# Performance work log

Hardware: AMD Instinct MI355X
Metric: run time of the kernel (lower is better)

Reference implementation:

```python
import jax, jax.numpy as jnp
import numpy as np

B, S, HID = 2, 2048, 4096
NH, NKV, D = 32, 8, 128  # heads, kv heads, head_dim
GROUPS = NH // NKV
THETA = 10000.0


def _rope_tables():
    inv_freq = 1.0 / (THETA ** (np.arange(0, D, 2, dtype=np.float32) / D))
    pos = np.arange(S, dtype=np.float32)
    freqs = pos[:, None] * inv_freq[None, :]          # [S, D/2]
    emb = np.concatenate([freqs, freqs], axis=-1)      # [S, D]
    cos = np.broadcast_to(np.cos(emb)[None], (B, S, D)).copy()
    sin = np.broadcast_to(np.sin(emb)[None], (B, S, D)).copy()
    return jnp.asarray(cos), jnp.asarray(sin)


def setup_inputs() -> dict:
    key = jax.random.key(0)
    ks = jax.random.split(key, 5)
    hidden_states = jax.random.normal(ks[0], (B, S, HID), dtype=jnp.float32)
    cos, sin = _rope_tables()
    std = 0.02
    Wq = jax.random.normal(ks[1], (NH * D, HID), dtype=jnp.float32) * std
    Wk = jax.random.normal(ks[2], (NKV * D, HID), dtype=jnp.float32) * std
    Wv = jax.random.normal(ks[3], (NKV * D, HID), dtype=jnp.float32) * std
    Wo = jax.random.normal(ks[4], (HID, NH * D), dtype=jnp.float32) * std
    return {"hidden_states": hidden_states, "cos": cos, "sin": sin,
            "Wq": Wq, "Wk": Wk, "Wv": Wv, "Wo": Wo}


def _rotate_half(x):
    x1, x2 = jnp.split(x, 2, axis=-1)
    return jnp.concatenate([-x2, x1], axis=-1)


def reference(hidden_states, cos, sin, Wq, Wk, Wv, Wo):
    b, s, _ = hidden_states.shape
    # QKV projections (no bias; attention_bias=False)
    q = (hidden_states @ Wq.T).reshape(b, s, NH, D).transpose(0, 2, 1, 3)    # [B,NH,S,D]
    k = (hidden_states @ Wk.T).reshape(b, s, NKV, D).transpose(0, 2, 1, 3)   # [B,NKV,S,D]
    v = (hidden_states @ Wv.T).reshape(b, s, NKV, D).transpose(0, 2, 1, 3)
    # RoPE (HF apply_rotary_pos_emb: cos/sin unsqueezed at head dim)
    c = cos[:, None, :, :]
    sn = sin[:, None, :, :]
    q = q * c + _rotate_half(q) * sn
    k = k * c + _rotate_half(k) * sn
    # GQA repeat_kv
    k = jnp.repeat(k, GROUPS, axis=1)                                        # [B,NH,S,D]
    v = jnp.repeat(v, GROUPS, axis=1)
    # dense evalmode: scores + causal mask + fp32 softmax
    scores = jnp.einsum('bhqd,bhkd->bhqk', q, k) / jnp.sqrt(jnp.float32(D))
    causal = jnp.triu(jnp.ones((s, s), dtype=bool), k=1)                     # True above diag
    scores = jnp.where(causal[None, None], jnp.float32(-jnp.inf), scores)
    attn = jax.nn.softmax(scores.astype(jnp.float32), axis=-1).astype(v.dtype)
    out = jnp.einsum('bhqk,bhkd->bhqd', attn, v)                             # [B,NH,S,D]
    out = out.transpose(0, 2, 1, 3).reshape(b, s, NH * D)
    return out @ Wo.T
```

## Files before the change

kernel.cpp:

```cpp
#include <hip/hip_runtime.h>
#include <hip/hip_bf16.h>

#define DEV __device__ __forceinline__

typedef __attribute__((ext_vector_type(8))) short bf16x8;
typedef __attribute__((ext_vector_type(4))) short s16x4;
typedef __attribute__((ext_vector_type(4))) float f32x4;

constexpr int B_ = 2, S_ = 2048, HID_ = 4096, NH_ = 32, NKV_ = 8, D_ = 128;
constexpr int GROUPS_ = NH_ / NKV_;
constexpr float QSCALE_ = 0.08838834764831845f * 1.4426950408889634f;

DEV unsigned short f2bf(float x) {
    union { float f; unsigned int u; } v; v.f = x;
    unsigned int r = v.u + 0x7fffu + ((v.u >> 16) & 1u);
    return (unsigned short)(r >> 16);
}

DEV f32x4 mfma16(bf16x8 a, bf16x8 b, f32x4 c) {
    return __builtin_amdgcn_mfma_f32_16x16x32_bf16(a, b, c, 0, 0, 0);
}

DEV void gll16(const void* g, void* l) {
    __builtin_amdgcn_global_load_lds(
        (const __attribute__((address_space(1))) unsigned int*)g,
        (__attribute__((address_space(3))) unsigned int*)l, 16, 0, 0);
}

__global__ __launch_bounds__(256) void cast_bf16_k(
    const float* __restrict__ src, unsigned short* __restrict__ dst, int n8)
{
    int i = blockIdx.x * 256 + threadIdx.x;
    if (i >= n8) return;
    const f32x4* s = (const f32x4*)(src + (size_t)i * 8);
    f32x4 a = s[0], b = s[1];
    bf16x8 o;
    o[0] = (short)f2bf(a[0]); o[1] = (short)f2bf(a[1]);
    o[2] = (short)f2bf(a[2]); o[3] = (short)f2bf(a[3]);
    o[4] = (short)f2bf(b[0]); o[5] = (short)f2bf(b[1]);
    o[6] = (short)f2bf(b[2]); o[7] = (short)f2bf(b[3]);
    *(bf16x8*)(dst + (size_t)i * 8) = o;
}

template<int EPI>
__global__ __launch_bounds__(512, 2) void gemm256_k(
    const unsigned short* __restrict__ A, const unsigned short* __restrict__ Bw,
    float* __restrict__ Cf,
    unsigned short* __restrict__ Qo, unsigned short* __restrict__ Ko,
    unsigned short* __restrict__ Vo,
    const float* __restrict__ cosT, const float* __restrict__ sinT,
    int M, int N, int K)
{
    __shared__ __align__(16) unsigned short lds[65536];
    const int tid = threadIdx.x, lane = tid & 63;
    const int w = tid >> 6, wm = w >> 2, wn = w & 3;
    const int la = lane & 15, lb = lane >> 4;

    const int nwg = (int)gridDim.x;
    const int cpx = nwg >> 3;
    const int bid = (int)blockIdx.x;
    const int sw = (bid & 7) * cpx + (bid >> 3);
    const int ntn = N >> 8;
    const int bm = (sw / ntn) << 8, bn = (sw % ntn) << 8;

    const int srow = tid >> 3;
    const int scol8 = (tid & 7) ^ (srow & 7);
    const size_t rK = (size_t)K;
    const unsigned short* gA = A + (size_t)(bm + srow) * rK + scol8 * 8;
    const unsigned short* gB = Bw + (size_t)(bn + srow) * rK + scol8 * 8;

#define STAGE_A_H0(buf, kt) { gll16(gA + (size_t)(kt),            &lds[(buf)*16384 + tid*8]); \
                              gll16(gA + (size_t)(kt) + 128*rK,   &lds[(buf)*16384 + 8192 + tid*8]); }
#define STAGE_A_H1(buf, kt) { gll16(gA + (size_t)(kt) + 64*rK,    &lds[(buf)*16384 + 4096 + tid*8]); \
                              gll16(gA + (size_t)(kt) + 192*rK,   &lds[(buf)*16384 + 12288 + tid*8]); }
#define STAGE_B_H0(buf, kt) { gll16(gB + (size_t)(kt),            &lds[32768 + (buf)*16384 + tid*8]); \
                              gll16(gB + (size_t)(kt) + 64*rK,    &lds[32768 + (buf)*16384 + 4096 + tid*8]); }
#define STAGE_B_H1(buf, kt) { gll16(gB + (size_t)(kt) + 128*rK,   &lds[32768 + (buf)*16384 + 8192 + tid*8]); \
                              gll16(gB + (size_t)(kt) + 192*rK,   &lds[32768 + (buf)*16384 + 12288 + tid*8]); }
#define SB0() __builtin_amdgcn_sched_barrier(0)

    f32x4 acc[8][4];
#pragma unroll
    for (int m = 0; m < 8; ++m)
#pragma unroll
        for (int j = 0; j < 4; ++j) acc[m][j] = f32x4{0.f, 0.f, 0.f, 0.f};

    auto rdA = [&](int buf, int m, int kk) -> bf16x8 {
        int r = wm * 128 + m * 16 + la;
        int slot = (kk * 4 + lb) ^ (la & 7);
        return *(const bf16x8*)&lds[buf * 16384 + r * 64 + slot * 8];
    };
    auto rdB = [&](int buf, int j, int kk) -> bf16x8 {
        int r = (wn + 4 * j) * 16 + la;
        int slot = (kk * 4 + lb) ^ (la & 7);
        return *(const bf16x8*)&lds[32768 + buf * 16384 + r * 64 + slot * 8];
    };

    STAGE_A_H0(0, 0); STAGE_B_H0(0, 0); STAGE_B_H1(0, 0); STAGE_A_H1(0, 0);

    bf16x8 af[4][2], b01[2][2], b23[2][2];
    int cur = 0;
    const int nt = K >> 6;
    for (int t = 0; t < nt; ++t) {
        const bool pre = (t + 1 < nt);
        const int kn = (t + 1) << 6;
        const int nb = cur ^ 1;
        asm volatile("s_waitcnt vmcnt(2)" ::: "memory");
        SB0(); __builtin_amdgcn_s_barrier(); SB0();
#pragma unroll
        for (int m = 0; m < 4; ++m)
#pragma unroll
            for (int kk = 0; kk < 2; ++kk) af[m][kk] = rdA(cur, m, kk);
#pragma unroll
        for (int j = 0; j < 2; ++j)
#pragma unroll
            for (int kk = 0; kk < 2; ++kk) b01[j][kk] = rdB(cur, j, kk);
        if (pre) STAGE_A_H0(nb, kn);
        __builtin_amdgcn_s_setprio(1);
#pragma unroll
        for (int kk = 0; kk < 2; ++kk)
#pragma unroll
            for (int m = 0; m < 4; ++m)
#pragma unroll
                for (int j = 0; j < 2; ++j)
                    acc[m][j] = mfma16(af[m][kk], b01[j][kk], acc[m][j]);
        __builtin_amdgcn_s_setprio(0);
        SB0(); __builtin_amdgcn_s_barrier(); SB0();
#pragma unroll
        for (int j = 0; j < 2; ++j)
#pragma unroll
            for (int kk = 0; kk < 2; ++kk) b23[j][kk] = rdB(cur, j + 2, kk);
        if (pre) STAGE_B_H0(nb, kn);
        __builtin_amdgcn_s_setprio(1);
#pragma unroll
        for (int kk = 0; kk < 2; ++kk)
#pragma unroll
            for (int m = 0; m < 4; ++m)
#pragma unroll
                for (int j = 0; j < 2; ++j)
                    acc[m][j + 2] = mfma16(af[m][kk], b23[j][kk], acc[m][j + 2]);
        __builtin_amdgcn_s_setprio(0);
        if (pre) { asm volatile("s_waitcnt vmcnt(4)" ::: "memory"); }
        else     { asm volatile("s_waitcnt vmcnt(0)" ::: "memory"); }
        SB0(); __builtin_amdgcn_s_barrier(); SB0();
#pragma unroll
        for (int m = 0; m < 4; ++m)
#pragma unroll
            for (int kk = 0; kk < 2; ++kk) af[m][kk] = rdA(cur, m + 4, kk);
        if (pre) STAGE_B_H1(nb, kn);
        __builtin_amdgcn_s_setprio(1);
#pragma unroll
        for (int kk = 0; kk < 2; ++kk)
#pragma unroll
            for (int m = 0; m < 4; ++m)
#pragma unroll
                for (int j = 0; j < 2; ++j)
                    acc[m + 4][j + 2] = mfma16(af[m][kk], b23[j][kk], acc[m + 4][j + 2]);
        __builtin_amdgcn_s_setprio(0);
        SB0(); __builtin_amdgcn_s_barrier(); SB0();
        if (pre) STAGE_A_H1(nb, kn);
        __builtin_amdgcn_s_setprio(1);
#pragma unroll
        for (int kk = 0; kk < 2; ++kk)
#pragma unroll
            for (int m = 0; m < 4; ++m)
#pragma unroll
                for (int j = 0; j < 2; ++j)
                    acc[m + 4][j] = mfma16(af[m][kk], b01[j][kk], acc[m + 4][j]);
        __builtin_amdgcn_s_setprio(0);
        cur ^= 1;
    }
#undef STAGE_A_H0
#undef STAGE_A_H1
#undef STAGE_B_H0
#undef STAGE_B_H1
#undef SB0

    const int srow0 = bm + wm * 128;
    if constexpr (EPI == 0) {
#pragma unroll
        for (int m = 0; m < 8; ++m)
#pragma unroll
            for (int j = 0; j < 4; ++j) {
                int col = bn + (wn + 4 * j) * 16 + la;
#pragma unroll
                for (int r = 0; r < 4; ++r)
                    Cf[(size_t)(srow0 + m * 16 + lb * 4 + r) * N + col] = acc[m][j][r];
            }
    } else {
        if (bn < 5120) {
            unsigned short* dst; int ld, hbase; float scale;
            if (bn < 4096) { dst = Qo; ld = NH_ * D_; hbase = bn >> 7; scale = QSCALE_; }
            else           { dst = Ko; ld = NKV_ * D_; hbase = (bn - 4096) >> 7; scale = 1.f; }
            const int d = wn * 16 + la;
#pragma unroll
            for (int m = 0; m < 8; ++m) {
#pragma unroll
                for (int r = 0; r < 4; ++r) {
                    int row = srow0 + m * 16 + lb * 4 + r;
                    float cv = cosT[(size_t)row * D_ + d];
                    float sv = sinT[(size_t)row * D_ + d];
#pragma unroll
                    for (int p = 0; p < 2; ++p) {
                        float x1 = acc[m][p * 2 + 0][r], x2 = acc[m][p * 2 + 1][r];
                        unsigned short* o = dst + (size_t)row * ld + (hbase + p) * D_ + d;
                        o[0]  = f2bf((x1 * cv - x2 * sv) * scale);
                        o[64] = f2bf((x2 * cv + x1 * sv) * scale);
                    }
                }
            }
        } else {
            const int col0 = bn - 5120;
#pragma unroll
            for (int m = 0; m < 8; ++m) {
                int row = srow0 + m * 16 + lb * 4;
                int b = row >> 11, s = row & (S_ - 1);
#pragma unroll
                for (int j = 0; j < 4; ++j) {
                    int c = col0 + (wn + 4 * j) * 16 + la;
                    int kv = c >> 7, d = c & 127;
                    s16x4 pk;
#pragma unroll
                    for (int r = 0; r < 4; ++r) pk[r] = (short)f2bf(acc[m][j][r]);
                    *(s16x4*)&Vo[((size_t)(b * NKV_ + kv) * D_ + d) * S_ + s] = pk;
                }
            }
        }
    }
}

template<int EPI, bool ABF16>
__global__ __launch_bounds__(256) void gemm_legacy_k(
    const void* __restrict__ Ap, const float* __restrict__ Bp,
    void* __restrict__ Cp, const float* __restrict__ cosT,
    const float* __restrict__ sinT, int M, int N, int K, float scale)
{
    constexpr int LDT = 40;
    __shared__ __align__(16) unsigned short Asm[128 * LDT];
    __shared__ __align__(16) unsigned short Bsm[128 * LDT];
    const int tid = threadIdx.x;
    const int lane = tid & 63;
    const int w = tid >> 6;
    const int la = lane & 15, lb = lane >> 4;
    const int ntn = N >> 7;
    const int bm = (int)(blockIdx.x / ntn) << 7;
    const int bn = (int)(blockIdx.x % ntn) << 7;

    f32x4 acc[2][8];
#pragma unroll
    for (int i = 0; i < 2; ++i)
#pragma unroll
        for (int j = 0; j < 8; ++j) acc[i][j] = f32x4{0.f, 0.f, 0.f, 0.f};

    for (int kt = 0; kt < K; kt += 32) {
        if constexpr (!ABF16) {
#pragma unroll
            for (int it = 0; it < 4; ++it) {
                int idx = it * 256 + tid;
                int r = idx >> 3, c = (idx & 7) << 2;
                const float* g = (const float*)Ap + (size_t)(bm + r) * K + kt + c;
                f32x4 v = *(const f32x4*)g;
                union { unsigned long long q; unsigned short u[4]; } pk;
                pk.u[0] = f2bf(v[0]); pk.u[1] = f2bf(v[1]);
                pk.u[2] = f2bf(v[2]); pk.u[3] = f2bf(v[3]);
                *(unsigned long long*)&Asm[r * LDT + c] = pk.q;
            }
        } else {
#pragma unroll
            for (int it = 0; it < 2; ++it) {
                int idx = it * 256 + tid;
                int r = idx >> 2, c = (idx & 3) << 3;
                const unsigned short* g =
                    (const unsigned short*)Ap + (size_t)(bm + r) * K + kt + c;
                *(bf16x8*)&Asm[r * LDT + c] = *(const bf16x8*)g;
            }
        }
#pragma unroll
        for (int it = 0; it < 4; ++it) {
            int idx = it * 256 + tid;
            int r = idx >> 3, c = (idx & 7) << 2;
            const float* g = Bp + (size_t)(bn + r) * K + kt + c;
            f32x4 v = *(const f32x4*)g;
            union { unsigned long long q; unsigned short u[4]; } pk;
            pk.u[0] = f2bf(v[0]); pk.u[1] = f2bf(v[1]);
            pk.u[2] = f2bf(v[2]); pk.u[3] = f2bf(v[3]);
            *(unsigned long long*)&Bsm[r * LDT + c] = pk.q;
        }
        __syncthreads();
        bf16x8 af0 = *(bf16x8*)&Asm[(w * 32 + la) * LDT + lb * 8];
        bf16x8 af1 = *(bf16x8*)&Asm[(w * 32 + 16 + la) * LDT + lb * 8];
#pragma unroll
        for (int nb = 0; nb < 8; ++nb) {
            bf16x8 bfr = *(bf16x8*)&Bsm[(nb * 16 + la) * LDT + lb * 8];
            acc[0][nb] = mfma16(af0, bfr, acc[0][nb]);
            acc[1][nb] = mfma16(af1, bfr, acc[1][nb]);
        }
        __syncthreads();
    }

    const int rbase = bm + w * 32;
    if constexpr (EPI == 0) {
        float* C = (float*)Cp;
#pragma unroll
        for (int mf = 0; mf < 2; ++mf)
#pragma unroll
            for (int nb = 0; nb < 8; ++nb)
#pragma unroll
                for (int r = 0; r < 4; ++r)
                    C[(size_t)(rbase + mf * 16 + lb * 4 + r) * N + bn + nb * 16 + la] =
                        acc[mf][nb][r];
    } else if constexpr (EPI == 1) {
        unsigned short* C = (unsigned short*)Cp;
#pragma unroll
        for (int mf = 0; mf < 2; ++mf) {
#pragma unroll
            for (int r = 0; r < 4; ++r) {
                int m = rbase + mf * 16 + lb * 4 + r;
                const float* cb = cosT + (size_t)m * D_;
                const float* sb = sinT + (size_t)m * D_;
#pragma unroll
                for (int nb = 0; nb < 4; ++nb) {
                    int d = nb * 16 + la;
                    float c = cb[d], s = sb[d];
                    float x1 = acc[mf][nb][r], x2 = acc[mf][nb + 4][r];
                    C[(size_t)m * N + bn + d]      = f2bf((x1 * c - x2 * s) * scale);
                    C[(size_t)m * N + bn + d + 64] = f2bf((x2 * c + x1 * s) * scale);
                }
            }
        }
    } else {
        unsigned short* C = (unsigned short*)Cp;
#pragma unroll
        for (int mf = 0; mf < 2; ++mf)
#pragma unroll
            for (int nb = 0; nb < 8; ++nb)
#pragma unroll
                for (int r = 0; r < 4; ++r) {
                    int m = rbase + mf * 16 + lb * 4 + r;
                    int b = m >> 11, s = m & (S_ - 1);
                    int n = bn + nb * 16 + la;
                    int kv = n >> 7, d = n & 127;
                    C[(((size_t)b * NKV_ + kv) * D_ + d) * S_ + s] =
                        f2bf(acc[mf][nb][r]);
                }
    }
}

__global__ __launch_bounds__(256, 2) void attn2_k(
    const unsigned short* __restrict__ Qw,
    const unsigned short* __restrict__ Kw,
    const unsigned short* __restrict__ Vt,
    unsigned short* __restrict__ Ow)
{
    constexpr int LDP = 72;
    __shared__ __align__(16) unsigned short Ksm[64 * 128];
    __shared__ __align__(16) unsigned short Vsm[128 * 64];
    __shared__ __align__(16) unsigned short Psm[4][32 * LDP];
    const int tid = threadIdx.x, lane = tid & 63, w = tid >> 6;
    const int la = lane & 15, lb = lane >> 4;
    const int blk = blockIdx.x;
    const int qbi = (S_ / 128 - 1) - (blk >> 6);
    const int bh = blk & 63;
    const int b = bh >> 5, h = bh & 31;
    const int kvh = h >> 2;
    const int qb = qbi * 128;
    const int qw0 = qb + w * 32;

    bf16x8 fq[2][4];
    const unsigned short* qp =
        Qw + ((size_t)(b * S_ + qw0 + la) * NH_ + h) * D_ + lb * 8;
#pragma unroll
    for (int mq = 0; mq < 2; ++mq)
#pragma unroll
        for (int kc = 0; kc < 4; ++kc)
            fq[mq][kc] = *(const bf16x8*)(qp + (size_t)mq * 16 * NH_ * D_ + kc * 32);

    float m_[2], l_[2];
    f32x4 oacc[8][2];
    m_[0] = m_[1] = -__builtin_inff();
    l_[0] = l_[1] = 0.f;
#pragma unroll
    for (int db = 0; db < 8; ++db)
#pragma unroll
        for (int mq = 0; mq < 2; ++mq) oacc[db][mq] = f32x4{0.f, 0.f, 0.f, 0.f};

    const int ntiles = (qb + 128) >> 6;
    for (int t = 0; t < ntiles; ++t) {
        const int kv0 = t << 6;
        {
            const int rb = tid >> 4, sl = tid & 15;
#pragma unroll
            for (int it = 0; it < 4; ++it) {
                int row = it * 16 + rb;
                int cc = sl ^ (row & 7);
                const unsigned short* g =
                    Kw + ((size_t)(b * S_ + kv0 + row) * NKV_ + kvh) * D_ + cc * 8;
                gll16(g, &Ksm[(it * 256 + tid) * 8]);
            }
        }
        {
            const int rb = tid >> 3, sl = tid & 7;
#pragma unroll
            for (int it = 0; it < 4; ++it) {
                int row = it * 32 + rb;
                int cc = sl ^ (row & 7);
                const unsigned short* g =
                    Vt + ((size_t)(b * NKV_ + kvh) * D_ + row) * S_ + kv0 + cc * 8;
                gll16(g, &Vsm[(it * 256 + tid) * 8]);
            }
        }
        __syncthreads();

        if (kv0 < qw0 + 32) {
            f32x4 sacc[4][2];
#pragma unroll
            for (int nk = 0; nk < 4; ++nk)
#pragma unroll
                for (int mq = 0; mq < 2; ++mq) sacc[nk][mq] = f32x4{0.f, 0.f, 0.f, 0.f};
#pragma unroll
            for (int kc = 0; kc < 4; ++kc) {
#pragma unroll
                for (int nk = 0; nk < 4; ++nk) {
                    int row = nk * 16 + la;
                    int slot = (kc * 4 + lb) ^ (la & 7);
                    bf16x8 fk = *(const bf16x8*)&Ksm[row * 128 + slot * 8];
#pragma unroll
                    for (int mq = 0; mq < 2; ++mq)
                        sacc[nk][mq] = mfma16(fk, fq[mq][kc], sacc[nk][mq]);
                }
            }
            const int qrow0 = qw0;
            float pv[4][2][4];
            float pm[2];
#pragma unroll
            for (int mq = 0; mq < 2; ++mq) {
                int q = qrow0 + mq * 16 + la;
                float mx = -__builtin_inff();
#pragma unroll
                for (int nk = 0; nk < 4; ++nk)
#pragma unroll
                    for (int r = 0; r < 4; ++r) {
                        int k = kv0 + nk * 16 + lb * 4 + r;
                        float s = (k <= q) ? sacc[nk][mq][r] : -__builtin_inff();
                        pv[nk][mq][r] = s;
                        mx = fmaxf(mx, s);
                    }
                mx = fmaxf(mx, __shfl_xor(mx, 16));
                mx = fmaxf(mx, __shfl_xor(mx, 32));
                pm[mq] = mx;
            }
            float fac[2], tsum[2];
#pragma unroll
            for (int mq = 0; mq < 2; ++mq) {
                float mn = fmaxf(m_[mq], pm[mq]);
                fac[mq] = exp2f(m_[mq] - mn);
                m_[mq] = mn;
                tsum[mq] = 0.f;
            }
#pragma unroll
            for (int nk = 0; nk < 4; ++nk)
#pragma unroll
                for (int mq = 0; mq < 2; ++mq)
#pragma unroll
                    for (int r = 0; r < 4; ++r) {
                        float p = exp2f(pv[nk][mq][r] - m_[mq]);
                        pv[nk][mq][r] = p;
                        tsum[mq] += p;
                    }
#pragma unroll
            for (int mq = 0; mq < 2; ++mq) {
                float s = tsum[mq];
                s += __shfl_xor(s, 16);
                s += __shfl_xor(s, 32);
                l_[mq] = l_[mq] * fac[mq] + s;
            }
#pragma unroll
            for (int db = 0; db < 8; ++db)
#pragma unroll
                for (int mq = 0; mq < 2; ++mq) oacc[db][mq] *= fac[mq];

            unsigned short* pp = &Psm[w][0];
#pragma unroll
            for (int nk = 0; nk < 4; ++nk)
#pragma unroll
                for (int mq = 0; mq < 2; ++mq) {
                    s16x4 pk;
#pragma unroll
                    for (int r = 0; r < 4; ++r) pk[r] = (short)f2bf(pv[nk][mq][r]);
                    *(s16x4*)&pp[(mq * 16 + la) * LDP + nk * 16 + lb * 4] = pk;
                }
            bf16x8 fp[2][2];
#pragma unroll
            for (int mq = 0; mq < 2; ++mq)
#pragma unroll
                for (int ks = 0; ks < 2; ++ks)
                    fp[mq][ks] =
                        *(const bf16x8*)&pp[(mq * 16 + la) * LDP + ks * 32 + lb * 8];
#pragma unroll
            for (int ks = 0; ks < 2; ++ks)
#pragma unroll
                for (int db = 0; db < 8; ++db) {
                    int row = db * 16 + la;
                    int slot = (ks * 4 + lb) ^ (la & 7);
                    bf16x8 fv = *(const bf16x8*)&Vsm[row * 64 + slot * 8];
#pragma unroll
                    for (int mq = 0; mq < 2; ++mq)
                        oacc[db][mq] = mfma16(fv, fp[mq][ks], oacc[db][mq]);
                }
        }
        __syncthreads();
    }

#pragma unroll
    for (int mq = 0; mq < 2; ++mq) {
        float rl = 1.f / l_[mq];
        int q = qw0 + mq * 16 + la;
#pragma unroll
        for (int db = 0; db < 8; ++db) {
            f32x4 o = oacc[db][mq];
            s16x4 pk;
#pragma unroll
            for (int r = 0; r < 4; ++r) pk[r] = (short)f2bf(o[r] * rl);
            int d = db * 16 + lb * 4;
            *(s16x4*)(Ow + (size_t)(b * S_ + q) * (NH_ * D_) + h * D_ + d) = pk;
        }
    }
}

extern "C" void kernel_launch(void* const* d_in, const int* in_sizes, int n_in,
                              void* d_out, int out_size, void* d_ws, size_t ws_size,
                              hipStream_t stream) {
    const float* hs   = (const float*)d_in[0];
    const float* cosT = (const float*)d_in[1];
    const float* sinT = (const float*)d_in[2];
    const float* Wq   = (const float*)d_in[3];
    const float* Wk   = (const float*)d_in[4];
    const float* Wv   = (const float*)d_in[5];
    const float* Wo   = (const float*)d_in[6];

    constexpr size_t Qn  = (size_t)B_ * S_ * NH_ * D_;
    constexpr size_t Kn  = (size_t)B_ * S_ * NKV_ * D_;
    constexpr size_t Hn  = (size_t)B_ * S_ * HID_;
    constexpr size_t Wqn = (size_t)NH_ * D_ * HID_;
    constexpr size_t Wkn = (size_t)NKV_ * D_ * HID_;

    unsigned short* Qws   = (unsigned short*)d_ws;
    unsigned short* Kws   = Qws + Qn;
    unsigned short* Vtws  = Kws + Kn;
    unsigned short* AOws  = Vtws + Kn;
    unsigned short* hsb   = AOws + Qn;
    unsigned short* Wqkvb = hsb + Hn;
    unsigned short* Wob   = Wqkvb + Wqn + 2 * Wkn;
    constexpr size_t need = (Qn + 2 * Kn + Qn + Hn + Wqn + 2 * Wkn + Wqn) * 2;

    const int M = B_ * S_;
    dim3 blk(256);

    if (ws_size >= need) {
        cast_bf16_k<<<dim3((int)(Hn / 8 / 256)), blk, 0, stream>>>(hs, hsb, (int)(Hn / 8));
        cast_bf16_k<<<dim3((int)(Wqn / 8 / 256)), blk, 0, stream>>>(Wq, Wqkvb, (int)(Wqn / 8));
        cast_bf16_k<<<dim3((int)(Wkn / 8 / 256)), blk, 0, stream>>>(Wk, Wqkvb + Wqn, (int)(Wkn / 8));
        cast_bf16_k<<<dim3((int)(Wkn / 8 / 256)), blk, 0, stream>>>(Wv, Wqkvb + Wqn + Wkn, (int)(Wkn / 8));
        cast_bf16_k<<<dim3((int)(Wqn / 8 / 256)), blk, 0, stream>>>(Wo, Wob, (int)(Wqn / 8));

        gemm256_k<1><<<dim3((M / 256) * (6144 / 256)), dim3(512), 0, stream>>>(
            hsb, Wqkvb, nullptr, Qws, Kws, Vtws, cosT, sinT, M, 6144, HID_);
        attn2_k<<<dim3(B_ * NH_ * (S_ / 128)), blk, 0, stream>>>(Qws, Kws, Vtws, AOws);
        gemm256_k<0><<<dim3((M / 256) * (HID_ / 256)), dim3(512), 0, stream>>>(
            AOws, Wob, (float*)d_out, nullptr, nullptr, nullptr, nullptr, nullptr,
            M, HID_, NH_ * D_);
    } else {
        unsigned short* Qf = (unsigned short*)d_ws;
        unsigned short* Kf = Qf + Qn;
        unsigned short* Vf = Kf + Kn;
        unsigned short* AOf = Vf + Kn;
        gemm_legacy_k<1, false><<<dim3((M / 128) * (NH_ * D_ / 128)), blk, 0, stream>>>(
            hs, Wq, Qf, cosT, sinT, M, NH_ * D_, HID_, QSCALE_);
        gemm_legacy_k<1, false><<<dim3((M / 128) * (NKV_ * D_ / 128)), blk, 0, stream>>>(
            hs, Wk, Kf, cosT, sinT, M, NKV_ * D_, HID_, 1.0f);
        gemm_legacy_k<3, false><<<dim3((M / 128) * (NKV_ * D_ / 128)), blk, 0, stream>>>(
            hs, Wv, Vf, nullptr, nullptr, M, NKV_ * D_, HID_, 0.f);
        attn2_k<<<dim3(B_ * NH_ * (S_ / 128)), blk, 0, stream>>>(Qf, Kf, Vf, AOf);
        gemm_legacy_k<0, true><<<dim3((M / 128) * (HID_ / 128)), blk, 0, stream>>>(
            AOf, Wo, (float*)d_out, nullptr, nullptr, M, HID_, NH_ * D_, 0.f);
    }
}
```

Measured before the change: 511.6 us.

## Merge casts, split K/V projection into separate GEMM, add lazy softmax rescaling

The five fp32-to-bf16 cast launches become one kernel that picks its source by block index. The fused QKV projection is split: the 256-tile GEMM now does only Q, and a new 128x128-tile kernel with higher occupancy handles K (with RoPE) and V (transposed). In attention, the causal mask is applied only on diagonal tiles, and the running max and accumulators are rescaled only when the max grows by more than a threshold (lazy rescale). This cuts launch overhead, wave-quantization tail in the QKV GEMM, and per-tile softmax work, but adds a launch and relies on the threshold to keep exp values bounded.

```diff
diff --git a/kernel.cpp b/kernel.cpp
--- a/kernel.cpp
+++ b/kernel.cpp
@@ -27,27 +27,36 @@
         (__attribute__((address_space(3))) unsigned int*)l, 16, 0, 0);
 }
 
-__global__ __launch_bounds__(256) void cast_bf16_k(
-    const float* __restrict__ src, unsigned short* __restrict__ dst, int n8)
+__global__ __launch_bounds__(256) void cast_all_k(
+    const float* __restrict__ s0, const float* __restrict__ s1,
+    const float* __restrict__ s2, const float* __restrict__ s3,
+    const float* __restrict__ s4,
+    unsigned short* __restrict__ d0, unsigned short* __restrict__ d1,
+    unsigned short* __restrict__ d2, unsigned short* __restrict__ d3,
+    unsigned short* __restrict__ d4)
 {
-    int i = blockIdx.x * 256 + threadIdx.x;
-    if (i >= n8) return;
-    const f32x4* s = (const f32x4*)(src + (size_t)i * 8);
-    f32x4 a = s[0], b = s[1];
+    int bb = blockIdx.x;
+    const float* s; unsigned short* d; int off;
+    if      (bb < 8192)  { s = s0; d = d0; off = bb; }
+    else if (bb < 16384) { s = s1; d = d1; off = bb - 8192; }
+    else if (bb < 18432) { s = s2; d = d2; off = bb - 16384; }
+    else if (bb < 20480) { s = s3; d = d3; off = bb - 18432; }
+    else                 { s = s4; d = d4; off = bb - 20480; }
+    size_t i = ((size_t)off * 256 + threadIdx.x) * 8;
+    const f32x4* sp = (const f32x4*)(s + i);
+    f32x4 a = sp[0], b = sp[1];
     bf16x8 o;
     o[0] = (short)f2bf(a[0]); o[1] = (short)f2bf(a[1]);
     o[2] = (short)f2bf(a[2]); o[3] = (short)f2bf(a[3]);
     o[4] = (short)f2bf(b[0]); o[5] = (short)f2bf(b[1]);
     o[6] = (short)f2bf(b[2]); o[7] = (short)f2bf(b[3]);
-    *(bf16x8*)(dst + (size_t)i * 8) = o;
+    *(bf16x8*)(d + i) = o;
 }
 
 template<int EPI>
 __global__ __launch_bounds__(512, 2) void gemm256_k(
     const unsigned short* __restrict__ A, const unsigned short* __restrict__ Bw,
-    float* __restrict__ Cf,
-    unsigned short* __restrict__ Qo, unsigned short* __restrict__ Ko,
-    unsigned short* __restrict__ Vo,
+    float* __restrict__ Cf, unsigned short* __restrict__ Qo,
     const float* __restrict__ cosT, const float* __restrict__ sinT,
     int M, int N, int K)
 {
@@ -174,7 +183,6 @@
 #undef STAGE_A_H1
 #undef STAGE_B_H0
 #undef STAGE_B_H1
-#undef SB0
 
     const int srow0 = bm + wm * 128;
     if constexpr (EPI == 0) {
@@ -188,42 +196,147 @@
                     Cf[(size_t)(srow0 + m * 16 + lb * 4 + r) * N + col] = acc[m][j][r];
             }
     } else {
-        if (bn < 5120) {
-            unsigned short* dst; int ld, hbase; float scale;
-            if (bn < 4096) { dst = Qo; ld = NH_ * D_; hbase = bn >> 7; scale = QSCALE_; }
-            else           { dst = Ko; ld = NKV_ * D_; hbase = (bn - 4096) >> 7; scale = 1.f; }
-            const int d = wn * 16 + la;
-#pragma unroll
-            for (int m = 0; m < 8; ++m) {
-#pragma unroll
-                for (int r = 0; r < 4; ++r) {
-                    int row = srow0 + m * 16 + lb * 4 + r;
-                    float cv = cosT[(size_t)row * D_ + d];
-                    float sv = sinT[(size_t)row * D_ + d];
-#pragma unroll
-                    for (int p = 0; p < 2; ++p) {
-                        float x1 = acc[m][p * 2 + 0][r], x2 = acc[m][p * 2 + 1][r];
-                        unsigned short* o = dst + (size_t)row * ld + (hbase + p) * D_ + d;
-                        o[0]  = f2bf((x1 * cv - x2 * sv) * scale);
-                        o[64] = f2bf((x2 * cv + x1 * sv) * scale);
-                    }
+        const int hbase = bn >> 7;
+        const int d = wn * 16 + la;
+#pragma unroll
+        for (int m = 0; m < 8; ++m) {
+#pragma unroll
+            for (int r = 0; r < 4; ++r) {
+                int row = srow0 + m * 16 + lb * 4 + r;
+                float cv = cosT[(size_t)row * D_ + d];
+                float sv = sinT[(size_t)row * D_ + d];
+#pragma unroll
+                for (int p = 0; p < 2; ++p) {
+                    float x1 = acc[m][p * 2 + 0][r], x2 = acc[m][p * 2 + 1][r];
+                    unsigned short* o = Qo + (size_t)row * (NH_ * D_) + (hbase + p) * D_ + d;
+                    o[0]  = f2bf((x1 * cv - x2 * sv) * QSCALE_);
+                    o[64] = f2bf((x2 * cv + x1 * sv) * QSCALE_);
                 }
             }
-        } else {
-            const int col0 = bn - 5120;
-#pragma unroll
-            for (int m = 0; m < 8; ++m) {
-                int row = srow0 + m * 16 + lb * 4;
-                int b = row >> 11, s = row & (S_ - 1);
-#pragma unroll
-                for (int j = 0; j < 4; ++j) {
-                    int c = col0 + (wn + 4 * j) * 16 + la;
-                    int kv = c >> 7, d = c & 127;
-                    s16x4 pk;
-#pragma unroll
-                    for (int r = 0; r < 4; ++r) pk[r] = (short)f2bf(acc[m][j][r]);
-                    *(s16x4*)&Vo[((size_t)(b * NKV_ + kv) * D_ + d) * S_ + s] = pk;
-                }
+        }
+    }
+}
+
+__global__ __launch_bounds__(512, 4) void gemm_kv_k(
+    const unsigned short* __restrict__ A, const unsigned short* __restrict__ Bw,
+    unsigned short* __restrict__ Ko, unsigned short* __restrict__ Vo,
+    const float* __restrict__ cosT, const float* __restrict__ sinT,
+    int M, int K)
+{
+    __shared__ __align__(16) unsigned short lds[32768];
+    const int tid = threadIdx.x, lane = tid & 63;
+    const int w = tid >> 6, wm = w >> 2, wn = w & 3;
+    const int la = lane & 15, lb = lane >> 4;
+
+    const int nwg = (int)gridDim.x;
+    const int cpx = nwg >> 3;
+    const int bid = (int)blockIdx.x;
+    const int sw = (bid & 7) * cpx + (bid >> 3);
+    const int ntn = 2048 >> 7;
+    const int bm = (sw / ntn) << 7, bn = (sw % ntn) << 7;
+
+    const int srow = tid >> 3;
+    const int scol8 = (tid & 7) ^ (srow & 7);
+    const size_t rK = (size_t)K;
+    const unsigned short* gA = A + (size_t)(bm + srow) * rK + scol8 * 8;
+    const unsigned short* gB = Bw + (size_t)(bn + srow) * rK + scol8 * 8;
+
+#define KV_STG_A(buf, kt)  { gll16(gA + (size_t)(kt),          &lds[(buf)*8192 + tid*8]); \
+                             gll16(gA + (size_t)(kt) + 64*rK,  &lds[(buf)*8192 + 4096 + tid*8]); }
+#define KV_STG_B0(buf, kt)   gll16(gB + (size_t)(kt),          &lds[16384 + (buf)*8192 + tid*8])
+#define KV_STG_B1(buf, kt)   gll16(gB + (size_t)(kt) + 64*rK,  &lds[16384 + (buf)*8192 + 4096 + tid*8])
+
+    f32x4 acc[4][2];
+#pragma unroll
+    for (int m = 0; m < 4; ++m)
+#pragma unroll
+        for (int j = 0; j < 2; ++j) acc[m][j] = f32x4{0.f, 0.f, 0.f, 0.f};
+
+    auto rdA = [&](int buf, int m, int kk) -> bf16x8 {
+        int r = wm * 64 + m * 16 + la;
+        int slot = (kk * 4 + lb) ^ (la & 7);
+        return *(const bf16x8*)&lds[buf * 8192 + r * 64 + slot * 8];
+    };
+    auto rdB = [&](int buf, int j, int kk) -> bf16x8 {
+        int r = (wn + 4 * j) * 16 + la;
+        int slot = (kk * 4 + lb) ^ (la & 7);
+        return *(const bf16x8*)&lds[16384 + buf * 8192 + r * 64 + slot * 8];
+    };
+
+    KV_STG_A(0, 0); KV_STG_B0(0, 0); KV_STG_B1(0, 0);
+
+    bf16x8 af[4][2], bf0[2], bf1[2];
+    int cur = 0;
+    const int nt = K >> 6;
+    for (int t = 0; t < nt; ++t) {
+        const bool pre = (t + 1 < nt);
+        const int kn = (t + 1) << 6;
+        const int nb = cur ^ 1;
+        asm volatile("s_waitcnt vmcnt(1)" ::: "memory");
+        SB0(); __builtin_amdgcn_s_barrier(); SB0();
+#pragma unroll
+        for (int m = 0; m < 4; ++m)
+#pragma unroll
+            for (int kk = 0; kk < 2; ++kk) af[m][kk] = rdA(cur, m, kk);
+#pragma unroll
+        for (int kk = 0; kk < 2; ++kk) bf0[kk] = rdB(cur, 0, kk);
+        if (pre) { KV_STG_A(nb, kn); KV_STG_B0(nb, kn); }
+        __builtin_amdgcn_s_setprio(1);
+#pragma unroll
+        for (int kk = 0; kk < 2; ++kk)
+#pragma unroll
+            for (int m = 0; m < 4; ++m)
+                acc[m][0] = mfma16(af[m][kk], bf0[kk], acc[m][0]);
+        __builtin_amdgcn_s_setprio(0);
+        if (pre) { asm volatile("s_waitcnt vmcnt(3)" ::: "memory"); }
+        else     { asm volatile("s_waitcnt vmcnt(0)" ::: "memory"); }
+        SB0(); __builtin_amdgcn_s_barrier(); SB0();
+#pragma unroll
+        for (int kk = 0; kk < 2; ++kk) bf1[kk] = rdB(cur, 1, kk);
+        if (pre) KV_STG_B1(nb, kn);
+        __builtin_amdgcn_s_setprio(1);
+#pragma unroll
+        for (int kk = 0; kk < 2; ++kk)
+#pragma unroll
+            for (int m = 0; m < 4; ++m)
+                acc[m][1] = mfma16(af[m][kk], bf1[kk], acc[m][1]);
+        __builtin_amdgcn_s_setprio(0);
+        cur ^= 1;
+    }
+#undef KV_STG_A
+#undef KV_STG_B0
+#undef KV_STG_B1
+#undef SB0
+
+    const int rbase = bm + wm * 64;
+    if (bn < 1024) {
+        const int hbase = bn >> 7;
+        const int d = wn * 16 + la;
+#pragma unroll
+        for (int m = 0; m < 4; ++m)
+#pragma unroll
+            for (int r = 0; r < 4; ++r) {
+                int row = rbase + m * 16 + lb * 4 + r;
+                float cv = cosT[(size_t)row * D_ + d];
+                float sv = sinT[(size_t)row * D_ + d];
+                float x1 = acc[m][0][r], x2 = acc[m][1][r];
+                unsigned short* o = Ko + (size_t)row * (NKV_ * D_) + hbase * D_ + d;
+                o[0]  = f2bf(x1 * cv - x2 * sv);
+                o[64] = f2bf(x2 * cv + x1 * sv);
+            }
+    } else {
+        const int kv = (bn - 1024) >> 7;
+#pragma unroll
+        for (int m = 0; m < 4; ++m) {
+            int row = rbase + m * 16 + lb * 4;
+            int b = row >> 11, s = row & (S_ - 1);
+#pragma unroll
+            for (int j = 0; j < 2; ++j) {
+                int d = (wn + 4 * j) * 16 + la;
+                s16x4 pk;
+#pragma unroll
+                for (int r = 0; r < 4; ++r) pk[r] = (short)f2bf(acc[m][j][r]);
+                *(s16x4*)&Vo[((size_t)(b * NKV_ + kv) * D_ + d) * S_ + s] = pk;
             }
         }
     }
@@ -429,19 +542,22 @@
                         sacc[nk][mq] = mfma16(fk, fq[mq][kc], sacc[nk][mq]);
                 }
             }
-            const int qrow0 = qw0;
+            const bool diag = (kv0 + 63 > qw0);
             float pv[4][2][4];
             float pm[2];
 #pragma unroll
             for (int mq = 0; mq < 2; ++mq) {
-                int q = qrow0 + mq * 16 + la;
+                int q = qw0 + mq * 16 + la;
                 float mx = -__builtin_inff();
 #pragma unroll
                 for (int nk = 0; nk < 4; ++nk)
 #pragma unroll
                     for (int r = 0; r < 4; ++r) {
-                        int k = kv0 + nk * 16 + lb * 4 + r;
-                        float s = (k <= q) ? sacc[nk][mq][r] : -__builtin_inff();
+                        float s = sacc[nk][mq][r];
+                        if (diag) {
+                            int k = kv0 + nk * 16 + lb * 4 + r;
+                            s = (k <= q) ? s : -__builtin_inff();
+                        }
                         pv[nk][mq][r] = s;
                         mx = fmaxf(mx, s);
                     }
@@ -449,14 +565,20 @@
                 mx = fmaxf(mx, __shfl_xor(mx, 32));
                 pm[mq] = mx;
             }
-            float fac[2], tsum[2];
-#pragma unroll
-            for (int mq = 0; mq < 2; ++mq) {
-                float mn = fmaxf(m_[mq], pm[mq]);
-                fac[mq] = exp2f(m_[mq] - mn);
-                m_[mq] = mn;
-                tsum[mq] = 0.f;
-            }
+            const bool upd =
+                __any((pm[0] > m_[0] + 8.f) || (pm[1] > m_[1] + 8.f));
+            if (upd) {
+#pragma unroll
+                for (int mq = 0; mq < 2; ++mq) {
+                    float mn = fmaxf(m_[mq], pm[mq]);
+                    float fac = exp2f(m_[mq] - mn);
+                    m_[mq] = mn;
+                    l_[mq] *= fac;
+#pragma unroll
+                    for (int db = 0; db < 8; ++db) oacc[db][mq] *= fac;
+                }
+            }
+            float tsum[2] = {0.f, 0.f};
 #pragma unroll
             for (int nk = 0; nk < 4; ++nk)
 #pragma unroll
@@ -472,12 +594,8 @@
                 float s = tsum[mq];
                 s += __shfl_xor(s, 16);
                 s += __shfl_xor(s, 32);
-                l_[mq] = l_[mq] * fac[mq] + s;
-            }
-#pragma unroll
-            for (int db = 0; db < 8; ++db)
-#pragma unroll
-                for (int mq = 0; mq < 2; ++mq) oacc[db][mq] *= fac[mq];
+                l_[mq] += s;
+            }
 
             unsigned short* pp = &Psm[w][0];
 #pragma unroll
@@ -557,18 +675,17 @@
     dim3 blk(256);
 
     if (ws_size >= need) {
-        cast_bf16_k<<<dim3((int)(Hn / 8 / 256)), blk, 0, stream>>>(hs, hsb, (int)(Hn / 8));
-        cast_bf16_k<<<dim3((int)(Wqn / 8 / 256)), blk, 0, stream>>>(Wq, Wqkvb, (int)(Wqn / 8));
-        cast_bf16_k<<<dim3((int)(Wkn / 8 / 256)), blk, 0, stream>>>(Wk, Wqkvb + Wqn, (int)(Wkn / 8));
-        cast_bf16_k<<<dim3((int)(Wkn / 8 / 256)), blk, 0, stream>>>(Wv, Wqkvb + Wqn + Wkn, (int)(Wkn / 8));
-        cast_bf16_k<<<dim3((int)(Wqn / 8 / 256)), blk, 0, stream>>>(Wo, Wob, (int)(Wqn / 8));
-
-        gemm256_k<1><<<dim3((M / 256) * (6144 / 256)), dim3(512), 0, stream>>>(
-            hsb, Wqkvb, nullptr, Qws, Kws, Vtws, cosT, sinT, M, 6144, HID_);
+        cast_all_k<<<dim3(28672), blk, 0, stream>>>(
+            hs, Wq, Wk, Wv, Wo,
+            hsb, Wqkvb, Wqkvb + Wqn, Wqkvb + Wqn + Wkn, Wob);
+
+        gemm256_k<1><<<dim3((M / 256) * (HID_ / 256)), dim3(512), 0, stream>>>(
+            hsb, Wqkvb, nullptr, Qws, cosT, sinT, M, HID_, HID_);
+        gemm_kv_k<<<dim3((M / 128) * (2048 / 128)), dim3(512), 0, stream>>>(
+            hsb, Wqkvb + Wqn, Kws, Vtws, cosT, sinT, M, HID_);
         attn2_k<<<dim3(B_ * NH_ * (S_ / 128)), blk, 0, stream>>>(Qws, Kws, Vtws, AOws);
         gemm256_k<0><<<dim3((M / 256) * (HID_ / 256)), dim3(512), 0, stream>>>(
-            AOws, Wob, (float*)d_out, nullptr, nullptr, nullptr, nullptr, nullptr,
-            M, HID_, NH_ * D_);
+            AOws, Wob, (float*)d_out, nullptr, nullptr, nullptr, M, HID_, NH_ * D_);
     } else {
         unsigned short* Qf = (unsigned short*)d_ws;
         unsigned short* Kf = Qf + Qn;
```

After: 479.5 us. -6.3%, faster.
